# Optimization experiments

Measured on AMD Instinct MI355X. Metric: run time of the kernel, lower is better.

## Reference

```python
import jax, jax.numpy as jnp
import numpy as np

T_ITERS = 10
EPS = 1e-5


def setup_inputs() -> dict:
    key = jax.random.key(0)
    B, C, H, W = 64, 256, 56, 56
    X = jax.random.normal(key, (B, C, H, W), dtype=jnp.float32)
    # running_rot buffer: orthogonal rotation per group (g=1)
    M = np.random.default_rng(0).standard_normal((C, C)).astype(np.float32)
    q, _ = np.linalg.qr(M)
    running_rot = jnp.asarray(q[None, :, :])  # [g=1, d, d]
    return {"X": X, "running_rot": running_rot}


def _whiten(X, g, nc):
    # X: [B, C, H, W] -> x: [g, d, m] with m = B*H*W (training-mode IterNorm)
    B, C, H, W = X.shape
    x = jnp.transpose(X, (1, 0, 2, 3)).reshape(g, nc, -1)
    m = x.shape[-1]
    mean = jnp.mean(x, axis=-1, keepdims=True)          # [g, d, 1]
    xc = x - mean                                        # [g, d, m]
    I = jnp.broadcast_to(jnp.eye(nc, dtype=X.dtype), (g, nc, nc))
    Sigma = EPS * I + jnp.matmul(xc, jnp.swapaxes(xc, 1, 2)) * (1.0 / m)
    # rTr = 1 / trace(Sigma) per group
    rTr = 1.0 / jnp.sum(Sigma * I, axis=(1, 2), keepdims=True)  # [g,1,1]
    Sigma_N = Sigma * rTr
    # Newton-Schulz iteration: P_{k+1} = 1.5 P_k - 0.5 P_k^3 Sigma_N
    P = I
    for _ in range(T_ITERS):
        P3 = jnp.matmul(jnp.matmul(P, P), P)
        P = 1.5 * P - 0.5 * jnp.matmul(P3, Sigma_N)
    wm = P * jnp.sqrt(rTr)                               # whitening matrix [g,d,d]
    xn = jnp.matmul(wm, xc)                              # [g, d, m]
    return xn.reshape(C, B, H, W).transpose(1, 0, 2, 3)  # back to [B,C,H,W]


def reference(X, running_rot):
    g, _, nc = running_rot.shape
    B, C, H, W = X.shape
    X_hat = _whiten(X, g, nc)                            # [B, C, H, W]
    Xg = X_hat.reshape(B, g, nc, H, W)
    # rotate whitened features: Q^T alignment, einsum('bgchw,gdc->bgdhw')
    Xr = jnp.einsum('bgchw,gdc->bgdhw', Xg, running_rot)
    return Xr.reshape(B, C, H, W)
```

## Files before the change

kernel.cpp:

```cpp
#include <hip/hip_runtime.h>
#include <math.h>

#define HWn   3136
#define Cn    256
#define KCPB  49
#define NCHUNK 3136
#define INV_M (1.0f/200704.0f)
#define EPSc  1e-5f

typedef __attribute__((ext_vector_type(4))) float f32x4;
typedef __attribute__((ext_vector_type(8))) short s16x8;
typedef __attribute__((ext_vector_type(4))) unsigned short u16x4;

static __device__ __forceinline__ unsigned short f2bf(float f) {
  unsigned int u = __builtin_bit_cast(unsigned int, f);
  u = (u + 0x7fffu + ((u >> 16) & 1u)) >> 16;
  return (unsigned short)u;
}

static __device__ __forceinline__ unsigned int cvt_pk_bf16(float lo, float hi) {
  unsigned int r;
  asm("v_cvt_pk_bf16_f32 %0, %1, %2" : "=v"(r) : "v"(lo), "v"(hi));
  return r;
}

__global__ __launch_bounds__(512) void k_gram(const float* __restrict__ X,
                                              float* __restrict__ Gp,
                                              float* __restrict__ Sp,
                                              float* __restrict__ Dp,
                                              int nparts) {
  __shared__ __align__(16) unsigned short lds[2][256 * 64];
  const int t = threadIdx.x, p = blockIdx.x;
  const int w = t >> 6, l = t & 63, a = l & 15, g = l >> 4;
  const int swzA = (a & 7) << 3;
  const int crow = t >> 1, h = t & 1;

  f32x4 acc[2][16];
#pragma unroll
  for (int rb = 0; rb < 2; ++rb)
#pragma unroll
    for (int j = 0; j < 16; ++j) acc[rb][j] = (f32x4){0.f, 0.f, 0.f, 0.f};
  float sumc = 0.f;
  float vx[32];

  const int start = (int)(((long)NCHUNK * p) / nparts);
  const int end   = (int)(((long)NCHUNK * (p + 1)) / nparts);

#define G_LOADS(CH)                                                           \
  {                                                                           \
    const int b_ = (CH) / KCPB, kc_ = (CH) % KCPB;                            \
    const float* xb_ = X + (long)b_ * Cn * HWn + kc_ * 64                     \
                         + (long)crow * HWn + h * 32;                         \
    _Pragma("unroll")                                                         \
    for (int q = 0; q < 8; ++q) {                                             \
      const float4 v = *(const float4*)(xb_ + q * 4);                         \
      vx[q * 4 + 0] = v.x; vx[q * 4 + 1] = v.y;                               \
      vx[q * 4 + 2] = v.z; vx[q * 4 + 3] = v.w;                               \
    }                                                                         \
  }

#define G_CVTWR(BUF)                                                          \
  {                                                                           \
    float s_ = 0.f;                                                           \
    _Pragma("unroll")                                                         \
    for (int q = 0; q < 8; ++q) {                                             \
      s_ += (vx[q * 4 + 0] + vx[q * 4 + 1]) + (vx[q * 4 + 2] + vx[q * 4 + 3]); \
      uint2 hh;                                                               \
      hh.x = cvt_pk_bf16(vx[q * 4 + 0], vx[q * 4 + 1]);                       \
      hh.y = cvt_pk_bf16(vx[q * 4 + 2], vx[q * 4 + 3]);                       \
      *(uint2*)(&lds[BUF][0] +                                                \
          ((crow * 64 + h * 32 + q * 4) ^ ((crow & 7) << 3))) = hh;           \
    }                                                                         \
    sumc += s_;                                                               \
  }

  G_LOADS(start);
  G_CVTWR(0);
  __syncthreads();

  for (int ch = start; ch < end; ++ch) {
    const int cur = (ch - start) & 1;
    if (ch + 1 < end) G_LOADS(ch + 1);
    const unsigned short* tile = &lds[cur][0];
    s16x8 fw[2][2];
#pragma unroll
    for (int rb = 0; rb < 2; ++rb)
#pragma unroll
      for (int kk2 = 0; kk2 < 2; ++kk2)
        fw[rb][kk2] = *(const s16x8*)(tile +
            ((((2 * w + rb) * 16 + a) * 64 + kk2 * 32 + g * 8) ^ swzA));
#pragma unroll
    for (int j = 0; j < 16; ++j) {
      const s16x8 fj0 = *(const s16x8*)(tile + (((j * 16 + a) * 64 + 0  + g * 8) ^ swzA));
      const s16x8 fj1 = *(const s16x8*)(tile + (((j * 16 + a) * 64 + 32 + g * 8) ^ swzA));
      acc[0][j] = __builtin_amdgcn_mfma_f32_16x16x32_bf16(fw[0][0], fj0, acc[0][j], 0, 0, 0);
      acc[0][j] = __builtin_amdgcn_mfma_f32_16x16x32_bf16(fw[0][1], fj1, acc[0][j], 0, 0, 0);
      acc[1][j] = __builtin_amdgcn_mfma_f32_16x16x32_bf16(fw[1][0], fj0, acc[1][j], 0, 0, 0);
      acc[1][j] = __builtin_amdgcn_mfma_f32_16x16x32_bf16(fw[1][1], fj1, acc[1][j], 0, 0, 0);
    }
    if (ch + 1 < end) G_CVTWR(cur ^ 1);
    __syncthreads();
  }
#undef G_LOADS
#undef G_CVTWR

  float* gout = Gp + (long)p * 65536;
#pragma unroll
  for (int rb = 0; rb < 2; ++rb)
#pragma unroll
    for (int j = 0; j < 16; ++j)
#pragma unroll
      for (int r = 0; r < 4; ++r)
        __builtin_nontemporal_store(acc[rb][j][r],
            gout + (32 * w + 16 * rb + 4 * g + r) * 256 + 16 * j + a);

  {
    const float so = __shfl_xor(sumc, 1);
    if ((t & 1) == 0) Sp[(long)p * 256 + crow] = sumc + so;
  }

  {
    float dsum = 0.f;
#pragma unroll
    for (int rb = 0; rb < 2; ++rb)
#pragma unroll
      for (int jj = 0; jj < 16; ++jj)
        if (jj == 2 * w + rb)
#pragma unroll
          for (int r = 0; r < 4; ++r)
            if (a == 4 * g + r) dsum += acc[rb][jj][r];
#pragma unroll
    for (int off = 1; off < 64; off <<= 1) dsum += __shfl_xor(dsum, off);
    float* lf = (float*)lds;
    __syncthreads();
    if (l == 0) lf[w] = dsum;
    __syncthreads();
    if (t == 0) {
      float d = 0.f;
#pragma unroll
      for (int ww = 0; ww < 8; ++ww) d += lf[ww];
      Dp[p] = d;
    }
  }
}

__global__ __launch_bounds__(1024) void k_reduce(const float* __restrict__ Gp,
                                                 const float* __restrict__ Sp,
                                                 const float* __restrict__ Dp,
                                                 float* __restrict__ Sigma,
                                                 float* __restrict__ P1,
                                                 float* __restrict__ meansum,
                                                 float* __restrict__ scal,
                                                 int nparts) {
  __shared__ float redA[4][256];
  __shared__ float msh[256];
  __shared__ float scrD[256];
  __shared__ float scrM[256];
  __shared__ __align__(16) float redB[16][256];
  const int t = threadIdx.x, j = blockIdx.x;
  const int c = t & 255, g = t >> 8;

  {
    float s = 0.f;
    const int pa0 = (nparts * g) >> 2, pa1 = (nparts * (g + 1)) >> 2;
    for (int p = pa0; p < pa1; ++p) s += Sp[(long)p * 256 + c];
    redA[g][c] = s;
  }
  __syncthreads();
  if (g == 0) msh[c] = (redA[0][c] + redA[1][c]) + (redA[2][c] + redA[3][c]);
  __syncthreads();

  if (t < 256) {
    scrD[t] = (t < nparts) ? Dp[t] : 0.f;
    const float mc = msh[t] * INV_M;
    scrM[t] = mc * mc;
  }
  __syncthreads();
  for (int st = 128; st > 0; st >>= 1) {
    if (t < st) { scrD[t] += scrD[t + st]; scrM[t] += scrM[t + st]; }
    __syncthreads();
  }
  const float tr = scrD[0] * INV_M - scrM[0] + 256.f * EPSc;
  const float rTr = 1.0f / tr;

  {
    const int c4 = (t & 63) * 4, sl = t >> 6;
    const int pb0 = (nparts * sl) >> 4, pb1 = (nparts * (sl + 1)) >> 4;
    const float* gp = Gp + (long)pb0 * 65536 + (long)j * 256 + c4;
    f32x4 s4 = (f32x4){0.f, 0.f, 0.f, 0.f};
    for (int p = pb0; p < pb1; ++p) {
      s4 += __builtin_nontemporal_load((const f32x4*)gp);
      gp += 65536;
    }
    *(f32x4*)&redB[sl][c4] = s4;
  }
  __syncthreads();

  if (t < 256) {
    float t0 = 0.f, t1 = 0.f;
#pragma unroll
    for (int sl = 0; sl < 16; sl += 2) { t0 += redB[sl][t]; t1 += redB[sl + 1][t]; }
    const float tot = t0 + t1;
    const float mc = msh[t] * INV_M;
    const float mj = msh[j] * INV_M;
    const float sig = tot * INV_M - mj * mc + ((j == t) ? EPSc : 0.f);
    Sigma[(long)j * 256 + t] = sig;
    P1[(long)j * 256 + t] = ((j == t) ? 1.5f : 0.f) - 0.5f * rTr * sig;
    if (j == 0) {
      meansum[t] = msh[t];
      if (t == 0) { scal[0] = tr; scal[1] = rTr; scal[2] = sqrtf(rTr); }
    }
  }
}

__global__ __launch_bounds__(1024) void k_ns(const float* __restrict__ Ps,
                                             float* __restrict__ Pd,
                                             const float* __restrict__ Sig,
                                             const float* __restrict__ scal) {
  __shared__ __align__(16) float PT[256][4];
  __shared__ __align__(16) float red[4][256][4];
  const int t = threadIdx.x, c = t & 255, kh = t >> 8, k0 = kh * 64;
  const int r0 = blockIdx.x * 4;

  PT[c][kh] = Ps[(r0 + kh) * 256 + c];
  __syncthreads();

  f32x4 acc;

#define NS_PHASE(BPTR)                                                        \
  {                                                                           \
    acc = (f32x4){0.f, 0.f, 0.f, 0.f};                                        \
    const float* Bb = (BPTR) + (long)k0 * 256 + c;                            \
    _Pragma("unroll 8")                                                       \
    for (int kk = 0; kk < 64; ++kk) {                                         \
      const float b = Bb[(long)kk * 256];                                     \
      const f32x4 a4 = *(const f32x4*)&PT[k0 + kk][0];                        \
      acc += a4 * b;                                                          \
    }                                                                         \
    *(f32x4*)&red[kh][c][0] = acc;                                            \
    __syncthreads();                                                          \
  }

#define NS_COMBINE()                                                          \
  {                                                                           \
    const f32x4 vs = (*(const f32x4*)&red[0][c][0] + *(const f32x4*)&red[1][c][0]) \
                   + (*(const f32x4*)&red[2][c][0] + *(const f32x4*)&red[3][c][0]); \
    if (kh == 0) *(f32x4*)&PT[c][0] = vs;                                     \
    __syncthreads();                                                          \
  }

  NS_PHASE(Ps);
  NS_COMBINE();
  NS_PHASE(Ps);
  NS_COMBINE();
  NS_PHASE(Sig);

  const float rTr = scal[1];
  const float t3 = ((red[0][c][kh] + red[1][c][kh]) + (red[2][c][kh] + red[3][c][kh]));
  const float pr = Ps[(r0 + kh) * 256 + c];
  Pd[(r0 + kh) * 256 + c] = 1.5f * pr - 0.5f * rTr * t3;
}

__global__ __launch_bounds__(1024) void k_ns_makeA(const float* __restrict__ Ps,
                                                   const float* __restrict__ Sig,
                                                   const float* __restrict__ rot,
                                                   const float* __restrict__ scal,
                                                   const float* __restrict__ meansum,
                                                   unsigned short* __restrict__ Abf,
                                                   float* __restrict__ bias) {
  __shared__ __align__(16) float PT[256][4];
  __shared__ __align__(16) float red[4][256][4];
  __shared__ float Tw[4][256];
  const int t = threadIdx.x, c = t & 255, kh = t >> 8, k0 = kh * 64;
  const int r0 = blockIdx.x * 4;

  PT[c][kh] = rot[(r0 + kh) * 256 + c];
  __syncthreads();

  f32x4 acc;

  NS_PHASE(Ps);
  NS_COMBINE();
  const float t1 = PT[c][kh];
  NS_PHASE(Ps);
  NS_COMBINE();
  NS_PHASE(Ps);
  NS_COMBINE();
  NS_PHASE(Sig);

  const float rTr = scal[1];
  const float sq = scal[2];
  const float t4 = (red[0][c][kh] + red[1][c][kh]) + (red[2][c][kh] + red[3][c][kh]);
  const float av = sq * (1.5f * t1 - 0.5f * rTr * t4);
  Abf[(r0 + kh) * 256 + c] = f2bf(av);
  const float mc = meansum[c] * INV_M;
  Tw[kh][c] = av * mc;
  __syncthreads();
  for (int st = 128; st > 0; st >>= 1) {
    if (c < st) Tw[kh][c] += Tw[kh][c + st];
    __syncthreads();
  }
  if (c == 0) bias[r0 + kh] = Tw[kh][0];
#undef NS_PHASE
#undef NS_COMBINE
}

__global__ __launch_bounds__(1024) void k_apply(const float* __restrict__ X,
                                                const unsigned short* __restrict__ Abf,
                                                const float* __restrict__ bias,
                                                float* __restrict__ out) {
  __shared__ __align__(16) unsigned short lds[2][64 * 256];
  const int t = threadIdx.x, w = t >> 6, l = t & 63, a = l & 15, g = l >> 4;
  const int bid = blockIdx.x;
  const int b = bid >> 3, strip = bid & 7;
  const int ch0 = (49 * strip) >> 3, ch1 = (49 * (strip + 1)) >> 3;

  const int d = 16 * w + a;
  s16x8 af[8];
#pragma unroll
  for (int kk8 = 0; kk8 < 8; ++kk8)
    af[kk8] = *(const s16x8*)(Abf + d * 256 + kk8 * 32 + g * 8);
  const float bd = bias[d];

  const float* xbase = X + (long)b * Cn * HWn;
  float* obase = out + (long)b * Cn * HWn;
  float vx[16];

#define A_LOADS(CH)                                                           \
  {                                                                           \
    const int s0_ = (CH) * 64;                                                \
    _Pragma("unroll")                                                         \
    for (int p4 = 0; p4 < 4; ++p4) {                                          \
      const int c4_ = p4 * 16 + w;                                            \
      const float* xp_ = xbase + (long)(c4_ * 4) * HWn + s0_ + l;             \
      vx[p4 * 4 + 0] = xp_[0];                                                \
      vx[p4 * 4 + 1] = xp_[HWn];                                              \
      vx[p4 * 4 + 2] = xp_[2 * HWn];                                          \
      vx[p4 * 4 + 3] = xp_[3 * HWn];                                          \
    }                                                                         \
  }

#define A_CVTWR(BUF)                                                          \
  {                                                                           \
    _Pragma("unroll")                                                         \
    for (int p4 = 0; p4 < 4; ++p4) {                                          \
      const int c4_ = p4 * 16 + w;                                            \
      uint2 hh;                                                               \
      hh.x = cvt_pk_bf16(vx[p4 * 4 + 0], vx[p4 * 4 + 1]);                     \
      hh.y = cvt_pk_bf16(vx[p4 * 4 + 2], vx[p4 * 4 + 3]);                     \
      *(uint2*)(&lds[BUF][0] + ((l * 256 + c4_ * 4) ^ ((l & 7) << 3))) = hh;  \
    }                                                                         \
  }

  A_LOADS(ch0);
  A_CVTWR(0);
  __syncthreads();

  for (int ch = ch0; ch < ch1; ++ch) {
    const int cur = (ch - ch0) & 1;
    if (ch + 1 < ch1) A_LOADS(ch + 1);

    const unsigned short* tile = &lds[cur][0];
    f32x4 acc[4];
#pragma unroll
    for (int st = 0; st < 4; ++st) acc[st] = (f32x4){0.f, 0.f, 0.f, 0.f};
#pragma unroll
    for (int kk8 = 0; kk8 < 8; ++kk8) {
#pragma unroll
      for (int st = 0; st < 4; ++st) {
        const s16x8 xf = *(const s16x8*)(tile + (((st * 16 + a) * 256 + kk8 * 32 + g * 8) ^ ((a & 7) << 3)));
        acc[st] = __builtin_amdgcn_mfma_f32_16x16x32_bf16(xf, af[kk8], acc[st], 0, 0, 0);
      }
    }
    const int s0 = ch * 64;
#pragma unroll
    for (int st = 0; st < 4; ++st) {
      const f32x4 o = acc[st] - bd;
      __builtin_nontemporal_store(o, (f32x4*)(obase + (long)d * HWn + s0 + st * 16 + 4 * g));
    }

    if (ch + 1 < ch1) A_CVTWR(cur ^ 1);
    __syncthreads();
  }
#undef A_LOADS
#undef A_CVTWR
}

extern "C" void kernel_launch(void* const* d_in, const int* in_sizes, int n_in,
                              void* d_out, int out_size, void* d_ws, size_t ws_size,
                              hipStream_t stream) {
  const float* X = (const float*)d_in[0];
  const float* rot = (const float*)d_in[1];
  float* out = (float*)d_out;

  auto need = [](int np) -> size_t {
    return (size_t)4 * ((size_t)np * 65536 + (size_t)np * 256 + (size_t)np
                        + 3 * 65536 + 256 + 16 + 256)
         + (size_t)2 * 65536;
  };
  int nparts = 256;
  while (nparts > 4 && need(nparts) > ws_size) nparts >>= 1;

  float* w = (float*)d_ws;
  float* Gp = w;       w += (size_t)nparts * 65536;
  float* Sp = w;       w += (size_t)nparts * 256;
  float* Dp = w;       w += (size_t)nparts;
  float* Sigma = w;    w += 65536;
  float* P0 = w;       w += 65536;
  float* P1 = w;       w += 65536;
  float* meansum = w;  w += 256;
  float* scal = w;     w += 16;
  float* bias = w;     w += 256;
  unsigned short* Abf = (unsigned short*)w;

  k_gram<<<dim3(nparts), dim3(512), 0, stream>>>(X, Gp, Sp, Dp, nparts);
  k_reduce<<<dim3(256), dim3(1024), 0, stream>>>(Gp, Sp, Dp, Sigma, P1, meansum, scal, nparts);
  float* ps = P1;
  float* pd = P0;
  for (int i = 0; i < 8; ++i) {
    k_ns<<<dim3(64), dim3(1024), 0, stream>>>(ps, pd, Sigma, scal);
    float* tmp = ps; ps = pd; pd = tmp;
  }
  k_ns_makeA<<<dim3(64), dim3(1024), 0, stream>>>(ps, Sigma, rot, scal, meansum, Abf, bias);
  k_apply<<<dim3(512), dim3(1024), 0, stream>>>(X, Abf, bias, out);
}
```

Baseline: 277.6 us.

## Exploit Gram symmetry: compute upper-triangle tiles only, atomics for mean/trace

```diff
diff --git a/kernel.cpp b/kernel.cpp
--- a/kernel.cpp
+++ b/kernel.cpp
@@ -26,14 +26,15 @@
 
 __global__ __launch_bounds__(512) void k_gram(const float* __restrict__ X,
                                               float* __restrict__ Gp,
-                                              float* __restrict__ Sp,
-                                              float* __restrict__ Dp,
+                                              float* __restrict__ meanacc,
+                                              float* __restrict__ gdt,
                                               int nparts) {
   __shared__ __align__(16) unsigned short lds[2][256 * 64];
   const int t = threadIdx.x, p = blockIdx.x;
   const int w = t >> 6, l = t & 63, a = l & 15, g = l >> 4;
   const int swzA = (a & 7) << 3;
   const int crow = t >> 1, h = t & 1;
+  const int R0 = w, R1 = 15 - w;
 
   f32x4 acc[2][16];
 #pragma unroll
@@ -82,21 +83,24 @@
     const int cur = (ch - start) & 1;
     if (ch + 1 < end) G_LOADS(ch + 1);
     const unsigned short* tile = &lds[cur][0];
-    s16x8 fw[2][2];
-#pragma unroll
-    for (int rb = 0; rb < 2; ++rb)
-#pragma unroll
-      for (int kk2 = 0; kk2 < 2; ++kk2)
-        fw[rb][kk2] = *(const s16x8*)(tile +
-            ((((2 * w + rb) * 16 + a) * 64 + kk2 * 32 + g * 8) ^ swzA));
+    s16x8 fw0[2], fw1[2];
+#pragma unroll
+    for (int kk2 = 0; kk2 < 2; ++kk2) {
+      fw0[kk2] = *(const s16x8*)(tile + (((R0 * 16 + a) * 64 + kk2 * 32 + g * 8) ^ swzA));
+      fw1[kk2] = *(const s16x8*)(tile + (((R1 * 16 + a) * 64 + kk2 * 32 + g * 8) ^ swzA));
+    }
 #pragma unroll
     for (int j = 0; j < 16; ++j) {
-      const s16x8 fj0 = *(const s16x8*)(tile + (((j * 16 + a) * 64 + 0  + g * 8) ^ swzA));
-      const s16x8 fj1 = *(const s16x8*)(tile + (((j * 16 + a) * 64 + 32 + g * 8) ^ swzA));
-      acc[0][j] = __builtin_amdgcn_mfma_f32_16x16x32_bf16(fw[0][0], fj0, acc[0][j], 0, 0, 0);
-      acc[0][j] = __builtin_amdgcn_mfma_f32_16x16x32_bf16(fw[0][1], fj1, acc[0][j], 0, 0, 0);
-      acc[1][j] = __builtin_amdgcn_mfma_f32_16x16x32_bf16(fw[1][0], fj0, acc[1][j], 0, 0, 0);
-      acc[1][j] = __builtin_amdgcn_mfma_f32_16x16x32_bf16(fw[1][1], fj1, acc[1][j], 0, 0, 0);
+      if (j >= R0) {
+        const s16x8 fj0 = *(const s16x8*)(tile + (((j * 16 + a) * 64 + 0  + g * 8) ^ swzA));
+        const s16x8 fj1 = *(const s16x8*)(tile + (((j * 16 + a) * 64 + 32 + g * 8) ^ swzA));
+        acc[0][j] = __builtin_amdgcn_mfma_f32_16x16x32_bf16(fw0[0], fj0, acc[0][j], 0, 0, 0);
+        acc[0][j] = __builtin_amdgcn_mfma_f32_16x16x32_bf16(fw0[1], fj1, acc[0][j], 0, 0, 0);
+        if (j >= R1) {
+          acc[1][j] = __builtin_amdgcn_mfma_f32_16x16x32_bf16(fw1[0], fj0, acc[1][j], 0, 0, 0);
+          acc[1][j] = __builtin_amdgcn_mfma_f32_16x16x32_bf16(fw1[1], fj1, acc[1][j], 0, 0, 0);
+        }
+      }
     }
     if (ch + 1 < end) G_CVTWR(cur ^ 1);
     __syncthreads();
@@ -105,30 +109,33 @@
 #undef G_CVTWR
 
   float* gout = Gp + (long)p * 65536;
-#pragma unroll
-  for (int rb = 0; rb < 2; ++rb)
-#pragma unroll
-    for (int j = 0; j < 16; ++j)
-#pragma unroll
-      for (int r = 0; r < 4; ++r)
-        __builtin_nontemporal_store(acc[rb][j][r],
-            gout + (32 * w + 16 * rb + 4 * g + r) * 256 + 16 * j + a);
+  float dsum = 0.f;
+#pragma unroll
+  for (int j = 0; j < 16; ++j) {
+    if (j >= R0) {
+#pragma unroll
+      for (int r = 0; r < 4; ++r) {
+        __builtin_nontemporal_store(acc[0][j][r],
+            gout + (16 * R0 + 4 * g + r) * 256 + 16 * j + a);
+        if (j == R0 && a == 4 * g + r) dsum += acc[0][j][r];
+      }
+    }
+    if (j >= R1) {
+#pragma unroll
+      for (int r = 0; r < 4; ++r) {
+        __builtin_nontemporal_store(acc[1][j][r],
+            gout + (16 * R1 + 4 * g + r) * 256 + 16 * j + a);
+        if (j == R1 && a == 4 * g + r) dsum += acc[1][j][r];
+      }
+    }
+  }
 
   {
     const float so = __shfl_xor(sumc, 1);
-    if ((t & 1) == 0) Sp[(long)p * 256 + crow] = sumc + so;
+    if (h == 0) atomicAdd(&meanacc[crow], sumc + so);
   }
 
   {
-    float dsum = 0.f;
-#pragma unroll
-    for (int rb = 0; rb < 2; ++rb)
-#pragma unroll
-      for (int jj = 0; jj < 16; ++jj)
-        if (jj == 2 * w + rb)
-#pragma unroll
-          for (int r = 0; r < 4; ++r)
-            if (a == 4 * g + r) dsum += acc[rb][jj][r];
 #pragma unroll
     for (int off = 1; off < 64; off <<= 1) dsum += __shfl_xor(dsum, off);
     float* lf = (float*)lds;
@@ -139,76 +146,67 @@
       float d = 0.f;
 #pragma unroll
       for (int ww = 0; ww < 8; ++ww) d += lf[ww];
-      Dp[p] = d;
-    }
-  }
-}
-
-__global__ __launch_bounds__(1024) void k_reduce(const float* __restrict__ Gp,
-                                                 const float* __restrict__ Sp,
-                                                 const float* __restrict__ Dp,
-                                                 float* __restrict__ Sigma,
-                                                 float* __restrict__ P1,
-                                                 float* __restrict__ meansum,
-                                                 float* __restrict__ scal,
-                                                 int nparts) {
-  __shared__ float redA[4][256];
+      atomicAdd(gdt, d);
+    }
+  }
+}
+
+__global__ __launch_bounds__(1024) void k_sigma(const float* __restrict__ Gp,
+                                                const float* __restrict__ meanacc,
+                                                const float* __restrict__ gdt,
+                                                float* __restrict__ Sigma,
+                                                float* __restrict__ P1,
+                                                float* __restrict__ scal,
+                                                int nparts) {
   __shared__ float msh[256];
-  __shared__ float scrD[256];
-  __shared__ float scrM[256];
-  __shared__ __align__(16) float redB[16][256];
-  const int t = threadIdx.x, j = blockIdx.x;
-  const int c = t & 255, g = t >> 8;
-
+  __shared__ float mu2s[256];
+  __shared__ __align__(16) float part[4][256];
+  const int t = threadIdx.x;
+
+  int i = 0, rem = blockIdx.x;
+  while (rem >= 16 - i) { rem -= 16 - i; ++i; }
+  const int j = i + rem;
+
+  if (t < 256) msh[t] = meanacc[t];
+  __syncthreads();
+  if (t < 256) { const float mc = msh[t] * INV_M; mu2s[t] = mc * mc; }
+  __syncthreads();
+  for (int st = 128; st > 0; st >>= 1) {
+    if (t < st) mu2s[t] += mu2s[t + st];
+    __syncthreads();
+  }
+  const float tr = gdt[0] * INV_M - mu2s[0] + 256.f * EPSc;
+  const float rTr = 1.0f / tr;
+
+  const int e = t & 255, sl = t >> 8;
+  const int r_ = e >> 4, c_ = e & 15;
+  const int psl = nparts >> 2;
   {
+    const float* gp = Gp + (long)(sl * psl) * 65536 + (16 * i + r_) * 256 + 16 * j + c_;
     float s = 0.f;
-    const int pa0 = (nparts * g) >> 2, pa1 = (nparts * (g + 1)) >> 2;
-    for (int p = pa0; p < pa1; ++p) s += Sp[(long)p * 256 + c];
-    redA[g][c] = s;
-  }
-  __syncthreads();
-  if (g == 0) msh[c] = (redA[0][c] + redA[1][c]) + (redA[2][c] + redA[3][c]);
-  __syncthreads();
-
-  if (t < 256) {
-    scrD[t] = (t < nparts) ? Dp[t] : 0.f;
-    const float mc = msh[t] * INV_M;
-    scrM[t] = mc * mc;
-  }
-  __syncthreads();
-  for (int st = 128; st > 0; st >>= 1) {
-    if (t < st) { scrD[t] += scrD[t + st]; scrM[t] += scrM[t + st]; }
-    __syncthreads();
-  }
-  const float tr = scrD[0] * INV_M - scrM[0] + 256.f * EPSc;
-  const float rTr = 1.0f / tr;
-
-  {
-    const int c4 = (t & 63) * 4, sl = t >> 6;
-    const int pb0 = (nparts * sl) >> 4, pb1 = (nparts * (sl + 1)) >> 4;
-    const float* gp = Gp + (long)pb0 * 65536 + (long)j * 256 + c4;
-    f32x4 s4 = (f32x4){0.f, 0.f, 0.f, 0.f};
-    for (int p = pb0; p < pb1; ++p) {
-      s4 += __builtin_nontemporal_load((const f32x4*)gp);
+    for (int p = 0; p < psl; ++p) {
+      s += __builtin_nontemporal_load(gp);
       gp += 65536;
     }
-    *(f32x4*)&redB[sl][c4] = s4;
-  }
-  __syncthreads();
-
-  if (t < 256) {
-    float t0 = 0.f, t1 = 0.f;
-#pragma unroll
-    for (int sl = 0; sl < 16; sl += 2) { t0 += redB[sl][t]; t1 += redB[sl + 1][t]; }
-    const float tot = t0 + t1;
-    const float mc = msh[t] * INV_M;
-    const float mj = msh[j] * INV_M;
-    const float sig = tot * INV_M - mj * mc + ((j == t) ? EPSc : 0.f);
-    Sigma[(long)j * 256 + t] = sig;
-    P1[(long)j * 256 + t] = ((j == t) ? 1.5f : 0.f) - 0.5f * rTr * sig;
-    if (j == 0) {
-      meansum[t] = msh[t];
-      if (t == 0) { scal[0] = tr; scal[1] = rTr; scal[2] = sqrtf(rTr); }
+    part[sl][e] = s;
+  }
+  __syncthreads();
+
+  if (sl == 0) {
+    const float gsum = (part[0][e] + part[1][e]) + (part[2][e] + part[3][e]);
+    const int row = 16 * i + r_, col = 16 * j + c_;
+    const float mur = msh[row] * INV_M;
+    const float muc = msh[col] * INV_M;
+    const float sig = gsum * INV_M - mur * muc + ((row == col) ? EPSc : 0.f);
+    const float p1v = ((row == col) ? 1.5f : 0.f) - 0.5f * rTr * sig;
+    Sigma[row * 256 + col] = sig;
+    P1[row * 256 + col] = p1v;
+    if (i != j) {
+      Sigma[col * 256 + row] = sig;
+      P1[col * 256 + row] = p1v;
+    }
+    if (blockIdx.x == 0 && e == 0) {
+      scal[0] = tr; scal[1] = rTr; scal[2] = sqrtf(rTr);
     }
   }
 }
@@ -265,7 +263,7 @@
                                                    const float* __restrict__ Sig,
                                                    const float* __restrict__ rot,
                                                    const float* __restrict__ scal,
-                                                   const float* __restrict__ meansum,
+                                                   const float* __restrict__ meanacc,
                                                    unsigned short* __restrict__ Abf,
                                                    float* __restrict__ bias) {
   __shared__ __align__(16) float PT[256][4];
@@ -293,7 +291,7 @@
   const float t4 = (red[0][c][kh] + red[1][c][kh]) + (red[2][c][kh] + red[3][c][kh]);
   const float av = sq * (1.5f * t1 - 0.5f * rTr * t4);
   Abf[(r0 + kh) * 256 + c] = f2bf(av);
-  const float mc = meansum[c] * INV_M;
+  const float mc = meanacc[c] * INV_M;
   Tw[kh][c] = av * mc;
   __syncthreads();
   for (int st = 128; st > 0; st >>= 1) {
@@ -394,33 +392,33 @@
   float* out = (float*)d_out;
 
   auto need = [](int np) -> size_t {
-    return (size_t)4 * ((size_t)np * 65536 + (size_t)np * 256 + (size_t)np
-                        + 3 * 65536 + 256 + 16 + 256)
+    return (size_t)4 * ((size_t)np * 65536 + 3 * 65536 + 256 + 16 + 16 + 256)
          + (size_t)2 * 65536;
   };
   int nparts = 256;
-  while (nparts > 4 && need(nparts) > ws_size) nparts >>= 1;
+  while (nparts > 8 && need(nparts) > ws_size) nparts >>= 1;
 
   float* w = (float*)d_ws;
   float* Gp = w;       w += (size_t)nparts * 65536;
-  float* Sp = w;       w += (size_t)nparts * 256;
-  float* Dp = w;       w += (size_t)nparts;
   float* Sigma = w;    w += 65536;
   float* P0 = w;       w += 65536;
   float* P1 = w;       w += 65536;
-  float* meansum = w;  w += 256;
+  float* meanacc = w;  w += 256;
+  float* gdt = w;      w += 16;
   float* scal = w;     w += 16;
   float* bias = w;     w += 256;
   unsigned short* Abf = (unsigned short*)w;
 
-  k_gram<<<dim3(nparts), dim3(512), 0, stream>>>(X, Gp, Sp, Dp, nparts);
-  k_reduce<<<dim3(256), dim3(1024), 0, stream>>>(Gp, Sp, Dp, Sigma, P1, meansum, scal, nparts);
+  hipMemsetAsync(meanacc, 0, (256 + 16) * sizeof(float), stream);
+
+  k_gram<<<dim3(nparts), dim3(512), 0, stream>>>(X, Gp, meanacc, gdt, nparts);
+  k_sigma<<<dim3(136), dim3(1024), 0, stream>>>(Gp, meanacc, gdt, Sigma, P1, scal, nparts);
   float* ps = P1;
   float* pd = P0;
   for (int i = 0; i < 8; ++i) {
     k_ns<<<dim3(64), dim3(1024), 0, stream>>>(ps, pd, Sigma, scal);
     float* tmp = ps; ps = pd; pd = tmp;
   }
-  k_ns_makeA<<<dim3(64), dim3(1024), 0, stream>>>(ps, Sigma, rot, scal, meansum, Abf, bias);
+  k_ns_makeA<<<dim3(64), dim3(1024), 0, stream>>>(ps, Sigma, rot, scal, meanacc, Abf, bias);
   k_apply<<<dim3(512), dim3(1024), 0, stream>>>(X, Abf, bias, out);
 }
```

Result: no change. 273.2 us (-1.6%).
